# Kernel tuning notes

Hardware: AMD Instinct MI355X
Metric: run time of the kernel (lower is better)

The kernel has to match this reference:

```python
import jax, jax.numpy as jnp
import numpy as np

N = 50000
E = 1600000
D_IN = 128
D_HID = 128
K = 16  # n_clusters


def spmm(edge_index, edge_weight, feats):
    # out[i] = sum_{(i<-j) in edges} w_e * feats[j]
    dst, src = edge_index[0], edge_index[1]
    msgs = feats[src] * edge_weight[:, None]  # [E, d]
    return jax.ops.segment_sum(msgs, dst, num_segments=N)


def gcn_with_skip(x, edge_index, edge_weight, W, b, skip_w):
    transformed = x @ W + b                      # Linear kernel
    propagated = spmm(edge_index, edge_weight, transformed)
    return jax.nn.selu(skip_w * transformed + propagated)


def setup_inputs() -> dict:
    key = jax.random.key(0)
    ks = jax.random.split(key, 12)
    x = jax.random.normal(ks[0], (N, D_IN), dtype=jnp.float32)
    edge_index = jax.random.randint(ks[1], (2, E), 0, N, dtype=jnp.int32)
    edge_weight = jax.random.uniform(ks[2], (E,), dtype=jnp.float32)
    s1 = 1.0 / np.sqrt(D_IN)
    s2 = 1.0 / np.sqrt(D_HID)
    W1 = jax.random.uniform(ks[3], (D_IN, D_HID), jnp.float32, -s1, s1)
    b1 = jax.random.uniform(ks[4], (D_HID,), jnp.float32, -s1, s1)
    skip1 = jnp.ones((D_HID,), jnp.float32)
    W2 = jax.random.uniform(ks[5], (D_HID, D_HID), jnp.float32, -s2, s2)
    b2 = jax.random.uniform(ks[6], (D_HID,), jnp.float32, -s2, s2)
    skip2 = jnp.ones((D_HID,), jnp.float32)
    Wa = jax.random.uniform(ks[7], (D_HID, K), jnp.float32, -s2, s2)
    ba = jax.random.uniform(ks[8], (K,), jnp.float32, -s2, s2)
    return {"x": x, "edge_index": edge_index, "edge_weight": edge_weight,
            "W1": W1, "b1": b1, "skip1": skip1,
            "W2": W2, "b2": b2, "skip2": skip2,
            "Wa": Wa, "ba": ba}


def reference(x, edge_index, edge_weight, W1, b1, skip1, W2, b2, skip2, Wa, ba):
    h = gcn_with_skip(x, edge_index, edge_weight, W1, b1, skip1)
    h = gcn_with_skip(h, edge_index, edge_weight, W2, b2, skip2)
    assignments = jax.nn.softmax(h @ Wa + ba, axis=-1)  # [N, K]
    return assignments
```

## Files before the change

### kernel.cpp

```cpp
#include <hip/hip_runtime.h>
#include <hip/hip_bf16.h>

#define NN 50000
#define NE 1600000
#define DD 128
#define KC 16

#define NB 1563
#define CHUNK 12288
#define NCHUNK 131
#define MAXB 1536

typedef __attribute__((ext_vector_type(8))) short s8v;
typedef __attribute__((ext_vector_type(4))) float f4v;

__device__ __forceinline__ float blo(unsigned u) { return __uint_as_float(u << 16); }
__device__ __forceinline__ float bhi(unsigned u) { return __uint_as_float(u & 0xFFFF0000u); }


__global__ __launch_bounds__(512) void k_bin(const int* __restrict__ dst,
                                             const int* __restrict__ src,
                                             const float* __restrict__ w,
                                             int* __restrict__ bcur,
                                             int2* __restrict__ staging) {
    __shared__ int h[NB];
    __shared__ int base[NB];
    int tid = threadIdx.x;
    for (int i = tid; i < NB; i += 512) h[i] = 0;
    __syncthreads();
    int cbase = blockIdx.x * CHUNK;
    for (int i = tid; i < CHUNK; i += 512) {
        int e = cbase + i;
        if (e < NE) atomicAdd(&h[dst[e] >> 5], 1);
    }
    __syncthreads();
    for (int i = tid; i < NB; i += 512) {
        int c = h[i];
        base[i] = c ? atomicAdd(&bcur[i], c) : 0;
    }
    __syncthreads();
    for (int i = tid; i < NB; i += 512) h[i] = 0;
    __syncthreads();
    for (int i = tid; i < CHUNK; i += 512) {
        int e = cbase + i;
        if (e < NE) {
            int d = dst[e];
            int b = d >> 5;
            int li = atomicAdd(&h[b], 1);
            int p = base[b] + li;
            if (p < MAXB) {
                int2 rec;
                rec.x = ((d & 31) << 16) | src[e];
                rec.y = __float_as_int(w[e]);
                staging[(size_t)b * MAXB + p] = rec;
            }
        }
    }
}


__global__ __launch_bounds__(256) void k_wprep(const float* __restrict__ W,
                                               s8v* __restrict__ Wf) {
    int g = blockIdx.x * 256 + threadIdx.x;
    int l = g & 63;
    int kcnt = g >> 6;
    int kc = kcnt >> 3, nt = kcnt & 7;
    int n = nt * 16 + (l & 15);
    int kb = kc * 32 + (l >> 4) * 8;
    union { s8v v; __hip_bfloat162 h2[4]; } u;
    #pragma unroll
    for (int q = 0; q < 4; q++) {
        float lo = W[(size_t)(kb + 2 * q) * 128 + n];
        float hi = W[(size_t)(kb + 2 * q + 1) * 128 + n];
        u.h2[q] = __float22bfloat162_rn(make_float2(lo, hi));
    }
    Wf[(size_t)kcnt * 64 + l] = u.v;
}


__global__ __launch_bounds__(256) void k_gemm_mfma(const float* __restrict__ X,
                                                   const s8v* __restrict__ Wf,
                                                   const float* __restrict__ bias,
                                                   __hip_bfloat16* __restrict__ Out,
                                                   int nrows) {
    int wave = blockIdx.x * 4 + (threadIdx.x >> 6);
    int lane = threadIdx.x & 63;
    int m0 = wave * 32;
    if (m0 >= nrows) return;
    int col = lane & 15;
    int quad = lane >> 4;

    f4v acc[2][8];
    #pragma unroll
    for (int mt = 0; mt < 2; mt++)
        #pragma unroll
        for (int nt = 0; nt < 8; nt++) acc[mt][nt] = (f4v){0.f, 0.f, 0.f, 0.f};

    int row0 = m0 + col;
    int row1 = m0 + 16 + col;
    if (row0 >= nrows) row0 = nrows - 1;
    if (row1 >= nrows) row1 = nrows - 1;
    const float* xr0 = X + (size_t)row0 * 128 + quad * 8;
    const float* xr1 = X + (size_t)row1 * 128 + quad * 8;

    #pragma unroll 1
    for (int kc = 0; kc < 4; kc++) {
        union { s8v v; __hip_bfloat162 h2[4]; } a0, a1;
        {
            float4 f0 = *(const float4*)(xr0 + kc * 32);
            float4 f1 = *(const float4*)(xr0 + kc * 32 + 4);
            a0.h2[0] = __float22bfloat162_rn(make_float2(f0.x, f0.y));
            a0.h2[1] = __float22bfloat162_rn(make_float2(f0.z, f0.w));
            a0.h2[2] = __float22bfloat162_rn(make_float2(f1.x, f1.y));
            a0.h2[3] = __float22bfloat162_rn(make_float2(f1.z, f1.w));
        }
        {
            float4 f0 = *(const float4*)(xr1 + kc * 32);
            float4 f1 = *(const float4*)(xr1 + kc * 32 + 4);
            a1.h2[0] = __float22bfloat162_rn(make_float2(f0.x, f0.y));
            a1.h2[1] = __float22bfloat162_rn(make_float2(f0.z, f0.w));
            a1.h2[2] = __float22bfloat162_rn(make_float2(f1.x, f1.y));
            a1.h2[3] = __float22bfloat162_rn(make_float2(f1.z, f1.w));
        }
        #pragma unroll
        for (int nt = 0; nt < 8; nt++) {
            s8v b = Wf[(size_t)(kc * 8 + nt) * 64 + lane];
            acc[0][nt] = __builtin_amdgcn_mfma_f32_16x16x32_bf16(a0.v, b, acc[0][nt], 0, 0, 0);
            acc[1][nt] = __builtin_amdgcn_mfma_f32_16x16x32_bf16(a1.v, b, acc[1][nt], 0, 0, 0);
        }
    }

    float bb[8];
    #pragma unroll
    for (int nt = 0; nt < 8; nt++) bb[nt] = bias[nt * 16 + col];

    #pragma unroll
    for (int mt = 0; mt < 2; mt++) {
        #pragma unroll
        for (int r = 0; r < 4; r++) {
            int row = m0 + mt * 16 + quad * 4 + r;
            if (row < nrows) {
                __hip_bfloat16* orow = Out + (size_t)row * 128 + col;
                #pragma unroll
                for (int nt = 0; nt < 8; nt++) {
                    orow[nt * 16] = __float2bfloat16(acc[mt][nt][r] + bb[nt]);
                }
            }
        }
    }
}


template <int ASSIGN>
__global__ __launch_bounds__(256) void k_spmm(const __hip_bfloat16* __restrict__ T,
                                              const int2* __restrict__ staging,
                                              const int* __restrict__ bcnt,
                                              const float* __restrict__ skip,
                                              float* __restrict__ Hout,
                                              const float* __restrict__ Wa,
                                              const float* __restrict__ ba,
                                              float* __restrict__ aout) {
    __shared__ int2 eord[MAXB + 8];
    __shared__ int rcnt[32];
    __shared__ int rowoff[33];
    int b = blockIdx.x;
    int tid = threadIdx.x;
    const int2* seg = staging + (size_t)b * MAXB;
    int cnt = bcnt[b];
    if (cnt > MAXB) cnt = MAXB;

    if (tid < 32) rcnt[tid] = 0;
    __syncthreads();
    for (int i = tid; i < cnt; i += 256) {
        int rib = ((unsigned)seg[i].x) >> 16;
        atomicAdd(&rcnt[rib], 1);
    }
    __syncthreads();
    if (tid < 32) {
        int v = rcnt[tid];
        int p = v;
        #pragma unroll
        for (int off = 1; off < 32; off <<= 1) {
            int u = __shfl_up(p, off, 64);
            if (tid >= off) p += u;
        }
        rowoff[tid] = p - v;
        if (tid == 31) rowoff[32] = p;
        rcnt[tid] = p - v;
    }
    __syncthreads();
    for (int i = tid; i < cnt; i += 256) {
        int2 rec = seg[i];
        int rib = ((unsigned)rec.x) >> 16;
        int p = atomicAdd(&rcnt[rib], 1);
        eord[p] = rec;
    }
    __syncthreads();
    if (tid < 8) eord[cnt + tid] = make_int2(0, 0);
    __syncthreads();

    int wv = tid >> 6, lane = tid & 63;
    int q = lane >> 4;
    int fk = lane & 15;
    const int4* Tv4 = (const int4*)T;

    float sk[8];
    *(float4*)&sk[0] = *(const float4*)(skip + fk * 8);
    *(float4*)&sk[4] = *(const float4*)(skip + fk * 8 + 4);

    float wreg[32];
    float bav[4];
    if (ASSIGN) {
        #pragma unroll
        for (int j = 0; j < 8; j++)
            *(float4*)&wreg[j * 4] = *(const float4*)(Wa + (size_t)(8 * fk + j) * KC + 4 * q);
        #pragma unroll
        for (int c = 0; c < 4; c++) bav[c] = ba[4 * q + c];
    }

    int nrows = NN - b * 32;
    if (nrows > 32) nrows = 32;
    const float scale = 1.0507009873554805f, alpha = 1.6732632423543772f;

    for (int r = wv; r < nrows; r += 4) {
        int g = b * 32 + r;
        int beg = rowoff[r], oe = rowoff[r + 1];
        float acc[8];
        #pragma unroll
        for (int j = 0; j < 8; j++) acc[j] = 0.f;

        int o = beg;
        for (; o + 8 <= oe; o += 8) {
            int2 ra = eord[o + q];
            int2 rb = eord[o + 4 + q];
            int4 ta = Tv4[(size_t)(ra.x & 0xFFFF) * 16 + fk];
            int4 tb = Tv4[(size_t)(rb.x & 0xFFFF) * 16 + fk];
            float wa_ = __int_as_float(ra.y);
            float wb_ = __int_as_float(rb.y);
            acc[0] += wa_ * blo(ta.x); acc[1] += wa_ * bhi(ta.x);
            acc[2] += wa_ * blo(ta.y); acc[3] += wa_ * bhi(ta.y);
            acc[4] += wa_ * blo(ta.z); acc[5] += wa_ * bhi(ta.z);
            acc[6] += wa_ * blo(ta.w); acc[7] += wa_ * bhi(ta.w);
            acc[0] += wb_ * blo(tb.x); acc[1] += wb_ * bhi(tb.x);
            acc[2] += wb_ * blo(tb.y); acc[3] += wb_ * bhi(tb.y);
            acc[4] += wb_ * blo(tb.z); acc[5] += wb_ * bhi(tb.z);
            acc[6] += wb_ * blo(tb.w); acc[7] += wb_ * bhi(tb.w);
        }
        for (; o < oe; o += 4) {
            int i0 = o + q;
            int2 ra = eord[i0];
            int4 ta = Tv4[(size_t)(ra.x & 0xFFFF) * 16 + fk];
            float wa_ = (i0 < oe) ? __int_as_float(ra.y) : 0.f;
            acc[0] += wa_ * blo(ta.x); acc[1] += wa_ * bhi(ta.x);
            acc[2] += wa_ * blo(ta.y); acc[3] += wa_ * bhi(ta.y);
            acc[4] += wa_ * blo(ta.z); acc[5] += wa_ * bhi(ta.z);
            acc[6] += wa_ * blo(ta.w); acc[7] += wa_ * bhi(ta.w);
        }

        #pragma unroll
        for (int j = 0; j < 8; j++) {
            acc[j] += __shfl_xor(acc[j], 16, 64);
            acc[j] += __shfl_xor(acc[j], 32, 64);
        }

        int4 ts = Tv4[(size_t)g * 16 + fk];
        float v[8];
        v[0] = sk[0] * blo(ts.x) + acc[0]; v[1] = sk[1] * bhi(ts.x) + acc[1];
        v[2] = sk[2] * blo(ts.y) + acc[2]; v[3] = sk[3] * bhi(ts.y) + acc[3];
        v[4] = sk[4] * blo(ts.z) + acc[4]; v[5] = sk[5] * bhi(ts.z) + acc[5];
        v[6] = sk[6] * blo(ts.w) + acc[6]; v[7] = sk[7] * bhi(ts.w) + acc[7];
        #pragma unroll
        for (int j = 0; j < 8; j++)
            v[j] = scale * (v[j] > 0.f ? v[j] : alpha * (__expf(v[j]) - 1.f));

        if (!ASSIGN) {
            if (q == 0) {
                float4* dp = (float4*)(Hout + (size_t)g * 128 + fk * 8);
                dp[0] = make_float4(v[0], v[1], v[2], v[3]);
                dp[1] = make_float4(v[4], v[5], v[6], v[7]);
            }
        } else {
            float p4[4] = {0.f, 0.f, 0.f, 0.f};
            #pragma unroll
            for (int j = 0; j < 8; j++)
                #pragma unroll
                for (int c = 0; c < 4; c++) p4[c] += v[j] * wreg[j * 4 + c];
            #pragma unroll
            for (int off = 1; off <= 8; off <<= 1)
                #pragma unroll
                for (int c = 0; c < 4; c++) p4[c] += __shfl_xor(p4[c], off, 64);
            #pragma unroll
            for (int c = 0; c < 4; c++) p4[c] += bav[c];
            float m = fmaxf(fmaxf(p4[0], p4[1]), fmaxf(p4[2], p4[3]));
            m = fmaxf(m, __shfl_xor(m, 16, 64));
            m = fmaxf(m, __shfl_xor(m, 32, 64));
            float e0 = __expf(p4[0] - m), e1 = __expf(p4[1] - m);
            float e2 = __expf(p4[2] - m), e3 = __expf(p4[3] - m);
            float s = e0 + e1 + e2 + e3;
            s += __shfl_xor(s, 16, 64);
            s += __shfl_xor(s, 32, 64);
            if (fk < 4) {
                float ev = e0;
                ev = (fk == 1) ? e1 : ev;
                ev = (fk == 2) ? e2 : ev;
                ev = (fk == 3) ? e3 : ev;
                aout[(size_t)g * KC + 4 * q + fk] = ev / s;
            }
        }
    }
}


extern "C" void kernel_launch(void* const* d_in, const int* in_sizes, int n_in,
                              void* d_out, int out_size, void* d_ws, size_t ws_size,
                              hipStream_t stream) {
    const float* x     = (const float*)d_in[0];
    const int*   eidx  = (const int*)d_in[1];
    const float* ew    = (const float*)d_in[2];
    const float* W1    = (const float*)d_in[3];
    const float* b1    = (const float*)d_in[4];
    const float* skip1 = (const float*)d_in[5];
    const float* W2    = (const float*)d_in[6];
    const float* b2    = (const float*)d_in[7];
    const float* skip2 = (const float*)d_in[8];
    const float* Wa    = (const float*)d_in[9];
    const float* ba    = (const float*)d_in[10];
    float* out = (float*)d_out;

    const int* dst = eidx;
    const int* src = eidx + NE;

    char* ws = (char*)d_ws;
    size_t off = 0;
    __hip_bfloat16* T = (__hip_bfloat16*)(ws + off); off += (size_t)NN * DD * 2;
    float* Hb = (float*)(ws + off);     off += (size_t)NN * DD * 4;
    int2* staging = (int2*)(ws + off);  off += (size_t)NB * MAXB * 8;
    int* bcur = (int*)(ws + off);       off += (size_t)NB * 4;
    s8v* Wf1 = (s8v*)(ws + off);        off += 2048 * 16;
    s8v* Wf2 = (s8v*)(ws + off);        off += 2048 * 16;

    hipMemsetAsync(bcur, 0, (size_t)NB * 4, stream);
    k_bin<<<NCHUNK, 512, 0, stream>>>(dst, src, ew, bcur, staging);

    k_wprep<<<8, 256, 0, stream>>>(W1, Wf1);
    k_wprep<<<8, 256, 0, stream>>>(W2, Wf2);

    int gemm_grid = (NN / 128) + 1;
    k_gemm_mfma<<<gemm_grid, 256, 0, stream>>>(x, Wf1, b1, T, NN);
    k_spmm<0><<<NB, 256, 0, stream>>>(T, staging, bcur, skip1, Hb, nullptr, nullptr, nullptr);
    k_gemm_mfma<<<gemm_grid, 256, 0, stream>>>(Hb, Wf2, b2, T, NN);
    k_spmm<1><<<NB, 256, 0, stream>>>(T, staging, bcur, skip2, nullptr, Wa, ba, out);
}
```

Baseline: 278.9 us.

## Precompute row-sorted CSR once with two-pass deterministic bin sort

Replaces the atomic-cursor binning with a two-stage sort. First, each chunk locally sorts its edges by destination bucket and records per-chunk offsets. Then a per-bucket kernel gathers those segments, sorts them by row in shared memory and writes a row pointer array. Both SpMM passes now read the row-ordered edges and rowptr straight from global memory instead of re-sorting in LDS, and the gather loop is unrolled to 16 edges. This adds a kernel launch and serial per-chunk copy loops, and reuses the Hb buffer as scratch.

```diff
diff --git a/kernel.cpp b/kernel.cpp
--- a/kernel.cpp
+++ b/kernel.cpp
@@ -7,8 +7,10 @@
 #define KC 16
 
 #define NB 1563
-#define CHUNK 12288
-#define NCHUNK 131
+#define NBP (NB + 1)
+#define CHUNK 6144
+#define NCHUNK 261
+#define EPT 12
 #define MAXB 1536
 
 typedef __attribute__((ext_vector_type(8))) short s8v;
@@ -18,44 +20,139 @@
 __device__ __forceinline__ float bhi(unsigned u) { return __uint_as_float(u & 0xFFFF0000u); }
 
 
-__global__ __launch_bounds__(512) void k_bin(const int* __restrict__ dst,
-                                             const int* __restrict__ src,
-                                             const float* __restrict__ w,
-                                             int* __restrict__ bcur,
-                                             int2* __restrict__ staging) {
-    __shared__ int h[NB];
-    __shared__ int base[NB];
-    int tid = threadIdx.x;
-    for (int i = tid; i < NB; i += 512) h[i] = 0;
-    __syncthreads();
-    int cbase = blockIdx.x * CHUNK;
-    for (int i = tid; i < CHUNK; i += 512) {
-        int e = cbase + i;
-        if (e < NE) atomicAdd(&h[dst[e] >> 5], 1);
-    }
-    __syncthreads();
-    for (int i = tid; i < NB; i += 512) {
-        int c = h[i];
-        base[i] = c ? atomicAdd(&bcur[i], c) : 0;
-    }
-    __syncthreads();
-    for (int i = tid; i < NB; i += 512) h[i] = 0;
-    __syncthreads();
-    for (int i = tid; i < CHUNK; i += 512) {
-        int e = cbase + i;
-        if (e < NE) {
-            int d = dst[e];
-            int b = d >> 5;
-            int li = atomicAdd(&h[b], 1);
-            int p = base[b] + li;
-            if (p < MAXB) {
-                int2 rec;
-                rec.x = ((d & 31) << 16) | src[e];
-                rec.y = __float_as_int(w[e]);
-                staging[(size_t)b * MAXB + p] = rec;
-            }
-        }
-    }
+__global__ __launch_bounds__(512) void k_binsort(const int* __restrict__ dst,
+                                                 const int* __restrict__ src,
+                                                 const float* __restrict__ w,
+                                                 int2* __restrict__ staging2,
+                                                 unsigned short* __restrict__ offs) {
+    __shared__ int cnt[NB];
+    __shared__ int s[512];
+    int t = threadIdx.x;
+    int c = blockIdx.x;
+    size_t cbase = (size_t)c * CHUNK;
+    for (int i = t; i < NB; i += 512) cnt[i] = 0;
+    __syncthreads();
+
+    int dreg[EPT], sreg[EPT]; float wreg[EPT];
+    #pragma unroll
+    for (int j = 0; j < EPT; j++) {
+        size_t e = cbase + j * 512 + t;
+        bool ok = e < NE;
+        size_t ee = ok ? e : (NE - 1);
+        dreg[j] = dst[ee]; sreg[j] = src[ee]; wreg[j] = w[ee];
+        if (!ok) dreg[j] = -1;
+        if (ok) atomicAdd(&cnt[dreg[j] >> 5], 1);
+    }
+    __syncthreads();
+
+    int v[4]; int sum = 0;
+    #pragma unroll
+    for (int j = 0; j < 4; j++) { int i = t * 4 + j; v[j] = (i < NB) ? cnt[i] : 0; sum += v[j]; }
+    s[t] = sum; __syncthreads();
+    for (int off = 1; off < 512; off <<= 1) {
+        int u = (t >= off) ? s[t - off] : 0;
+        __syncthreads();
+        s[t] += u;
+        __syncthreads();
+    }
+    int run = (t == 0) ? 0 : s[t - 1];
+    #pragma unroll
+    for (int j = 0; j < 4; j++) {
+        int i = t * 4 + j;
+        if (i < NB) { offs[(size_t)c * NBP + i] = (unsigned short)run; cnt[i] = run; run += v[j]; }
+    }
+    if (t == 511) offs[(size_t)c * NBP + NB] = (unsigned short)s[511];
+    __syncthreads();
+
+    #pragma unroll
+    for (int j = 0; j < EPT; j++) {
+        if (dreg[j] >= 0) {
+            int b = dreg[j] >> 5;
+            int li = atomicAdd(&cnt[b], 1);
+            staging2[cbase + li] = make_int2(((dreg[j] & 31) << 16) | sreg[j],
+                                            __float_as_int(wreg[j]));
+        }
+    }
+}
+
+
+__global__ __launch_bounds__(256) void k_rowsort(const int2* __restrict__ staging2,
+                                                 const unsigned short* __restrict__ offs,
+                                                 int2* __restrict__ staging,
+                                                 int* __restrict__ rowptr) {
+    __shared__ int2 ebuf[MAXB];
+    __shared__ int2 ebuf2[MAXB];
+    __shared__ int segoff[NCHUNK];
+    __shared__ int cstart[NCHUNK];
+    __shared__ int s2[256];
+    __shared__ int rcnt[32];
+    __shared__ int rowoff[33];
+    int b = blockIdx.x, t = threadIdx.x;
+
+    for (int c = t; c < NCHUNK; c += 256) {
+        int o0 = offs[(size_t)c * NBP + b];
+        int o1 = offs[(size_t)c * NBP + b + 1];
+        cstart[c] = o0;
+        segoff[c] = o1 - o0;
+    }
+    __syncthreads();
+    int a0 = (2 * t < NCHUNK) ? segoff[2 * t] : 0;
+    int a1 = (2 * t + 1 < NCHUNK) ? segoff[2 * t + 1] : 0;
+    s2[t] = a0 + a1; __syncthreads();
+    for (int off = 1; off < 256; off <<= 1) {
+        int u = (t >= off) ? s2[t - off] : 0;
+        __syncthreads();
+        s2[t] += u;
+        __syncthreads();
+    }
+    int base0 = (t == 0) ? 0 : s2[t - 1];
+    int total = s2[255];
+    __syncthreads();
+    if (2 * t < NCHUNK) segoff[2 * t] = base0;
+    if (2 * t + 1 < NCHUNK) segoff[2 * t + 1] = base0 + a0;
+    __syncthreads();
+
+    int cnt = total; if (cnt > MAXB) cnt = MAXB;
+
+    for (int c = t; c < NCHUNK; c += 256) {
+        int so = segoff[c], st = cstart[c];
+        int o1 = offs[(size_t)c * NBP + b + 1];
+        const int2* sp = staging2 + (size_t)c * CHUNK + st;
+        int len = o1 - st;
+        for (int j = 0; j < len; j++) {
+            int p = so + j;
+            if (p < MAXB) ebuf[p] = sp[j];
+        }
+    }
+    __syncthreads();
+
+    if (t < 32) rcnt[t] = 0;
+    __syncthreads();
+    for (int i = t; i < cnt; i += 256) atomicAdd(&rcnt[(unsigned)ebuf[i].x >> 16], 1);
+    __syncthreads();
+    if (t < 32) {
+        int v = rcnt[t];
+        int p = v;
+        #pragma unroll
+        for (int off = 1; off < 32; off <<= 1) {
+            int u = __shfl_up(p, off, 64);
+            if (t >= off) p += u;
+        }
+        rowoff[t] = p - v;
+        if (t == 31) rowoff[32] = p;
+        rcnt[t] = p - v;
+    }
+    __syncthreads();
+    for (int i = t; i < cnt; i += 256) {
+        int2 rec = ebuf[i];
+        int p = atomicAdd(&rcnt[(unsigned)rec.x >> 16], 1);
+        ebuf2[p] = rec;
+    }
+    __syncthreads();
+
+    int2* outp = staging + (size_t)b * MAXB;
+    for (int i = t; i < cnt; i += 256) outp[i] = ebuf2[i];
+    if (t < 33) rowptr[b * 33 + t] = rowoff[t];
 }
 
 
@@ -154,54 +251,18 @@
 template <int ASSIGN>
 __global__ __launch_bounds__(256) void k_spmm(const __hip_bfloat16* __restrict__ T,
                                               const int2* __restrict__ staging,
-                                              const int* __restrict__ bcnt,
+                                              const int* __restrict__ rowptr,
                                               const float* __restrict__ skip,
                                               float* __restrict__ Hout,
                                               const float* __restrict__ Wa,
                                               const float* __restrict__ ba,
                                               float* __restrict__ aout) {
-    __shared__ int2 eord[MAXB + 8];
-    __shared__ int rcnt[32];
-    __shared__ int rowoff[33];
     int b = blockIdx.x;
     int tid = threadIdx.x;
-    const int2* seg = staging + (size_t)b * MAXB;
-    int cnt = bcnt[b];
-    if (cnt > MAXB) cnt = MAXB;
-
-    if (tid < 32) rcnt[tid] = 0;
-    __syncthreads();
-    for (int i = tid; i < cnt; i += 256) {
-        int rib = ((unsigned)seg[i].x) >> 16;
-        atomicAdd(&rcnt[rib], 1);
-    }
-    __syncthreads();
-    if (tid < 32) {
-        int v = rcnt[tid];
-        int p = v;
-        #pragma unroll
-        for (int off = 1; off < 32; off <<= 1) {
-            int u = __shfl_up(p, off, 64);
-            if (tid >= off) p += u;
-        }
-        rowoff[tid] = p - v;
-        if (tid == 31) rowoff[32] = p;
-        rcnt[tid] = p - v;
-    }
-    __syncthreads();
-    for (int i = tid; i < cnt; i += 256) {
-        int2 rec = seg[i];
-        int rib = ((unsigned)rec.x) >> 16;
-        int p = atomicAdd(&rcnt[rib], 1);
-        eord[p] = rec;
-    }
-    __syncthreads();
-    if (tid < 8) eord[cnt + tid] = make_int2(0, 0);
-    __syncthreads();
-
     int wv = tid >> 6, lane = tid & 63;
     int q = lane >> 4;
     int fk = lane & 15;
+    const int2* seg = staging + (size_t)b * MAXB;
     const int4* Tv4 = (const int4*)T;
 
     float sk[8];
@@ -224,37 +285,64 @@
 
     for (int r = wv; r < nrows; r += 4) {
         int g = b * 32 + r;
-        int beg = rowoff[r], oe = rowoff[r + 1];
+        int o = rowptr[b * 33 + r];
+        int oe = rowptr[b * 33 + r + 1];
         float acc[8];
         #pragma unroll
         for (int j = 0; j < 8; j++) acc[j] = 0.f;
 
-        int o = beg;
+        for (; o + 16 <= oe; o += 16) {
+            int2 r0 = seg[o + q];
+            int2 r1 = seg[o + 4 + q];
+            int2 r2 = seg[o + 8 + q];
+            int2 r3 = seg[o + 12 + q];
+            int4 t0 = Tv4[(size_t)(r0.x & 0xFFFF) * 16 + fk];
+            int4 t1 = Tv4[(size_t)(r1.x & 0xFFFF) * 16 + fk];
+            int4 t2 = Tv4[(size_t)(r2.x & 0xFFFF) * 16 + fk];
+            int4 t3 = Tv4[(size_t)(r3.x & 0xFFFF) * 16 + fk];
+            float w0 = __int_as_float(r0.y), w1 = __int_as_float(r1.y);
+            float w2 = __int_as_float(r2.y), w3 = __int_as_float(r3.y);
+            acc[0] += w0 * blo(t0.x); acc[1] += w0 * bhi(t0.x);
+            acc[2] += w0 * blo(t0.y); acc[3] += w0 * bhi(t0.y);
+            acc[4] += w0 * blo(t0.z); acc[5] += w0 * bhi(t0.z);
+            acc[6] += w0 * blo(t0.w); acc[7] += w0 * bhi(t0.w);
+            acc[0] += w1 * blo(t1.x); acc[1] += w1 * bhi(t1.x);
+            acc[2] += w1 * blo(t1.y); acc[3] += w1 * bhi(t1.y);
+            acc[4] += w1 * blo(t1.z); acc[5] += w1 * bhi(t1.z);
+            acc[6] += w1 * blo(t1.w); acc[7] += w1 * bhi(t1.w);
+            acc[0] += w2 * blo(t2.x); acc[1] += w2 * bhi(t2.x);
+            acc[2] += w2 * blo(t2.y); acc[3] += w2 * bhi(t2.y);
+            acc[4] += w2 * blo(t2.z); acc[5] += w2 * bhi(t2.z);
+            acc[6] += w2 * blo(t2.w); acc[7] += w2 * bhi(t2.w);
+            acc[0] += w3 * blo(t3.x); acc[1] += w3 * bhi(t3.x);
+            acc[2] += w3 * blo(t3.y); acc[3] += w3 * bhi(t3.y);
+            acc[4] += w3 * blo(t3.z); acc[5] += w3 * bhi(t3.z);
+            acc[6] += w3 * blo(t3.w); acc[7] += w3 * bhi(t3.w);
+        }
         for (; o + 8 <= oe; o += 8) {
-            int2 ra = eord[o + q];
-            int2 rb = eord[o + 4 + q];
-            int4 ta = Tv4[(size_t)(ra.x & 0xFFFF) * 16 + fk];
-            int4 tb = Tv4[(size_t)(rb.x & 0xFFFF) * 16 + fk];
-            float wa_ = __int_as_float(ra.y);
-            float wb_ = __int_as_float(rb.y);
-            acc[0] += wa_ * blo(ta.x); acc[1] += wa_ * bhi(ta.x);
-            acc[2] += wa_ * blo(ta.y); acc[3] += wa_ * bhi(ta.y);
-            acc[4] += wa_ * blo(ta.z); acc[5] += wa_ * bhi(ta.z);
-            acc[6] += wa_ * blo(ta.w); acc[7] += wa_ * bhi(ta.w);
-            acc[0] += wb_ * blo(tb.x); acc[1] += wb_ * bhi(tb.x);
-            acc[2] += wb_ * blo(tb.y); acc[3] += wb_ * bhi(tb.y);
-            acc[4] += wb_ * blo(tb.z); acc[5] += wb_ * bhi(tb.z);
-            acc[6] += wb_ * blo(tb.w); acc[7] += wb_ * bhi(tb.w);
+            int2 r0 = seg[o + q];
+            int2 r1 = seg[o + 4 + q];
+            int4 t0 = Tv4[(size_t)(r0.x & 0xFFFF) * 16 + fk];
+            int4 t1 = Tv4[(size_t)(r1.x & 0xFFFF) * 16 + fk];
+            float w0 = __int_as_float(r0.y), w1 = __int_as_float(r1.y);
+            acc[0] += w0 * blo(t0.x); acc[1] += w0 * bhi(t0.x);
+            acc[2] += w0 * blo(t0.y); acc[3] += w0 * bhi(t0.y);
+            acc[4] += w0 * blo(t0.z); acc[5] += w0 * bhi(t0.z);
+            acc[6] += w0 * blo(t0.w); acc[7] += w0 * bhi(t0.w);
+            acc[0] += w1 * blo(t1.x); acc[1] += w1 * bhi(t1.x);
+            acc[2] += w1 * blo(t1.y); acc[3] += w1 * bhi(t1.y);
+            acc[4] += w1 * blo(t1.z); acc[5] += w1 * bhi(t1.z);
+            acc[6] += w1 * blo(t1.w); acc[7] += w1 * bhi(t1.w);
         }
         for (; o < oe; o += 4) {
             int i0 = o + q;
-            int2 ra = eord[i0];
-            int4 ta = Tv4[(size_t)(ra.x & 0xFFFF) * 16 + fk];
-            float wa_ = (i0 < oe) ? __int_as_float(ra.y) : 0.f;
-            acc[0] += wa_ * blo(ta.x); acc[1] += wa_ * bhi(ta.x);
-            acc[2] += wa_ * blo(ta.y); acc[3] += wa_ * bhi(ta.y);
-            acc[4] += wa_ * blo(ta.z); acc[5] += wa_ * bhi(ta.z);
-            acc[6] += wa_ * blo(ta.w); acc[7] += wa_ * bhi(ta.w);
+            int2 r0 = seg[i0];
+            int4 t0 = Tv4[(size_t)(r0.x & 0xFFFF) * 16 + fk];
+            float w0 = (i0 < oe) ? __int_as_float(r0.y) : 0.f;
+            acc[0] += w0 * blo(t0.x); acc[1] += w0 * bhi(t0.x);
+            acc[2] += w0 * blo(t0.y); acc[3] += w0 * bhi(t0.y);
+            acc[4] += w0 * blo(t0.z); acc[5] += w0 * bhi(t0.z);
+            acc[6] += w0 * blo(t0.w); acc[7] += w0 * bhi(t0.w);
         }
 
         #pragma unroll
@@ -333,21 +421,23 @@
     char* ws = (char*)d_ws;
     size_t off = 0;
     __hip_bfloat16* T = (__hip_bfloat16*)(ws + off); off += (size_t)NN * DD * 2;
-    float* Hb = (float*)(ws + off);     off += (size_t)NN * DD * 4;
-    int2* staging = (int2*)(ws + off);  off += (size_t)NB * MAXB * 8;
-    int* bcur = (int*)(ws + off);       off += (size_t)NB * 4;
-    s8v* Wf1 = (s8v*)(ws + off);        off += 2048 * 16;
-    s8v* Wf2 = (s8v*)(ws + off);        off += 2048 * 16;
-
-    hipMemsetAsync(bcur, 0, (size_t)NB * 4, stream);
-    k_bin<<<NCHUNK, 512, 0, stream>>>(dst, src, ew, bcur, staging);
+    float* Hb = (float*)(ws + off);                  off += (size_t)NN * DD * 4;
+    int2* staging2 = (int2*)Hb;
+    int2* staging = (int2*)(ws + off);               off += ((size_t)NB * MAXB + 16) * 8;
+    unsigned short* offs = (unsigned short*)(ws + off); off += (size_t)NCHUNK * NBP * 2;
+    int* rowptr = (int*)(ws + off);                  off += (size_t)NB * 33 * 4;
+    s8v* Wf1 = (s8v*)(ws + off);                     off += 2048 * 16;
+    s8v* Wf2 = (s8v*)(ws + off);                     off += 2048 * 16;
+
+    k_binsort<<<NCHUNK, 512, 0, stream>>>(dst, src, ew, staging2, offs);
+    k_rowsort<<<NB, 256, 0, stream>>>(staging2, offs, staging, rowptr);
 
     k_wprep<<<8, 256, 0, stream>>>(W1, Wf1);
     k_wprep<<<8, 256, 0, stream>>>(W2, Wf2);
 
     int gemm_grid = (NN / 128) + 1;
     k_gemm_mfma<<<gemm_grid, 256, 0, stream>>>(x, Wf1, b1, T, NN);
-    k_spmm<0><<<NB, 256, 0, stream>>>(T, staging, bcur, skip1, Hb, nullptr, nullptr, nullptr);
+    k_spmm<0><<<NB, 256, 0, stream>>>(T, staging, rowptr, skip1, Hb, nullptr, nullptr, nullptr);
     k_gemm_mfma<<<gemm_grid, 256, 0, stream>>>(Hb, Wf2, b2, T, NN);
-    k_spmm<1><<<NB, 256, 0, stream>>>(T, staging, bcur, skip2, nullptr, Wa, ba, out);
-}
+    k_spmm<1><<<NB, 256, 0, stream>>>(T, staging, rowptr, skip2, nullptr, Wa, ba, out);
+}
```

Result: slower. 301.9 us (+8.3%).
